# Optimization experiments

Measured on AMD Instinct MI355X. Metric: run time of the kernel, lower is better.

The kernel has to match this reference:

```python
import jax, jax.numpy as jnp
import numpy as np
from math import sqrt, ceil

OUTPUT_DIM = 50257
INPUT_DIM = 1024
N_CLASSES = int(ceil(sqrt(OUTPUT_DIM)))            # 225
N_OUT_PER_CLASS = int(ceil(OUTPUT_DIM / N_CLASSES))  # 224


def setup_inputs() -> dict:
    key = jax.random.key(0)
    k_x, k_w1, k_w2 = jax.random.split(key, 3)
    X = jax.random.normal(k_x, (8, 128, INPUT_DIM), dtype=jnp.float32)
    # glorot-ish scale so softmax logits stay in a sane range
    s1 = float(np.sqrt(2.0 / (INPUT_DIM + N_CLASSES)))
    s2 = float(np.sqrt(2.0 / (INPUT_DIM + N_OUT_PER_CLASS)))
    W1 = jax.random.normal(k_w1, (INPUT_DIM, N_CLASSES), dtype=jnp.float32) * s1
    b1 = jnp.zeros((N_CLASSES,), dtype=jnp.float32)
    W2 = jax.random.normal(k_w2, (N_CLASSES, INPUT_DIM, N_OUT_PER_CLASS), dtype=jnp.float32) * s2
    b2 = jnp.zeros((N_CLASSES, N_OUT_PER_CLASS), dtype=jnp.float32)
    return {"X": X, "W1": W1, "b1": b1, "W2": W2, "b2": b2}


def reference(X, W1, b1, W2, b2):
    """Two-level hierarchical softmax, inference path (target=None).

    P(y) = softmax(x@W1+b1)[class(y)] * softmax(x@W2[class(y)]+b2[class(y)])[offset(y)]
    Computed densely over all classes and flattened to the full vocab.
    """
    B, L, D = X.shape
    x = X.reshape(-1, D)                                    # [N, D], N = B*L
    class_probs = jax.nn.softmax(x @ W1 + b1, axis=-1)      # [N, C]
    # per-class logits: [N, C, O]
    acts = jnp.einsum('nd,cdo->nco', x, W2) + b2
    within = jax.nn.softmax(acts, axis=-1)                  # [N, C, O]
    probs = within * class_probs[:, :, None]                # [N, C, O]
    probs = probs.reshape(x.shape[0], N_CLASSES * N_OUT_PER_CLASS)[:, :OUTPUT_DIM]
    return probs.reshape(B, L, OUTPUT_DIM)
```

## Files before the change

### kernel.cpp

```cpp
#include <hip/hip_runtime.h>
#include <hip/hip_bf16.h>

#define CLS 225
#define OPC 224
#define DIM 1024
#define NTOK 1024
#define VOCAB 50257

#define BM 128
#define BK 32
#define NT 14

typedef __attribute__((ext_vector_type(8))) short bf16x8;
typedef __attribute__((ext_vector_type(4))) float f32x4;

__device__ __forceinline__ unsigned short f2bf(float f) {
  unsigned u = __float_as_uint(f);
  u += 0x7FFFu + ((u >> 16) & 1u);
  return (unsigned short)(u >> 16);
}

__device__ __forceinline__ void gll16(const void* gsrc, void* ldst) {
  __builtin_amdgcn_global_load_lds(
      (const __attribute__((address_space(1))) void*)gsrc,
      (__attribute__((address_space(3))) void*)ldst, 16, 0, 0);
}

__global__ __launch_bounds__(256) void hs_cls_fused(
    const float* __restrict__ X, const float* __restrict__ W1,
    const float* __restrict__ b1, float* __restrict__ cls,
    unsigned short* __restrict__ Xws)
{
  const int r0 = blockIdx.x * 4;
  const int tid = threadIdx.x;

  __shared__ float xs[4][DIM];
  __shared__ float lg[4][CLS];

  {
    const float4* src = (const float4*)(X + (size_t)r0 * DIM);
    float4* dst = (float4*)xs;
    for (int i = tid; i < 4 * DIM / 4; i += 256) dst[i] = src[i];
  }
  __syncthreads();

  for (int i = tid; i < 512; i += 256) {
    const int r = i >> 7, grp = i & 127;
    const int t = grp >> 2, slot = grp & 3;
    const int n = r0 + r;
    const float* p = &xs[r][t * 32 + slot * 8];
    bf16x8 pk;
#pragma unroll
    for (int j = 0; j < 8; ++j) pk[j] = (short)f2bf(p[j]);
    const int wb = (n * 64 + slot * 16) ^ ((n & 7) << 4);
    *(bf16x8*)((char*)Xws + (size_t)t * 65536 + wb) = pk;
  }

  if (tid < CLS) {
    float acc0 = 0.f, acc1 = 0.f, acc2 = 0.f, acc3 = 0.f;
    const float* w1p = W1 + tid;
    for (int d = 0; d < DIM; d += 8) {
      float w[8];
#pragma unroll
      for (int u = 0; u < 8; ++u) w[u] = w1p[(size_t)(d + u) * CLS];
#pragma unroll
      for (int u = 0; u < 8; ++u) {
        acc0 += xs[0][d + u] * w[u];
        acc1 += xs[1][d + u] * w[u];
        acc2 += xs[2][d + u] * w[u];
        acc3 += xs[3][d + u] * w[u];
      }
    }
    const float bb = b1[tid];
    lg[0][tid] = acc0 + bb;
    lg[1][tid] = acc1 + bb;
    lg[2][tid] = acc2 + bb;
    lg[3][tid] = acc3 + bb;
  }
  __syncthreads();

  const int wave = tid >> 6, lane = tid & 63;
  {
    const int r = wave;
    float v[4];
    float m = -1e30f;
#pragma unroll
    for (int i = 0; i < 4; ++i) {
      const int c2 = lane + i * 64;
      v[i] = (c2 < CLS) ? lg[r][c2] : -1e30f;
      m = fmaxf(m, v[i]);
    }
#pragma unroll
    for (int mask = 32; mask >= 1; mask >>= 1) m = fmaxf(m, __shfl_xor(m, mask));
    float e[4];
    float s = 0.f;
#pragma unroll
    for (int i = 0; i < 4; ++i) {
      const int c2 = lane + i * 64;
      e[i] = (c2 < CLS) ? __expf(v[i] - m) : 0.f;
      s += e[i];
    }
#pragma unroll
    for (int mask = 32; mask >= 1; mask >>= 1) s += __shfl_xor(s, mask);
    const float inv = 1.f / s;
#pragma unroll
    for (int i = 0; i < 4; ++i) {
      const int c2 = lane + i * 64;
      if (c2 < CLS) cls[(size_t)(r0 + r) * CLS + c2] = e[i] * inv;
    }
  }
}

__global__ __launch_bounds__(256) void hs_cls_kernel(
    const float* __restrict__ X, const float* __restrict__ W1,
    const float* __restrict__ b1, float* __restrict__ cls)
{
  const int r0 = blockIdx.x * 4;
  const int tid = threadIdx.x;

  __shared__ float xs[4][DIM];
  __shared__ float lg[4][CLS];

  {
    const float4* src = (const float4*)(X + (size_t)r0 * DIM);
    float4* dst = (float4*)xs;
    for (int i = tid; i < 4 * DIM / 4; i += 256) dst[i] = src[i];
  }
  __syncthreads();

  if (tid < CLS) {
    float acc0 = 0.f, acc1 = 0.f, acc2 = 0.f, acc3 = 0.f;
    const float* w1p = W1 + tid;
    for (int d = 0; d < DIM; d += 8) {
      float w[8];
#pragma unroll
      for (int u = 0; u < 8; ++u) w[u] = w1p[(size_t)(d + u) * CLS];
#pragma unroll
      for (int u = 0; u < 8; ++u) {
        acc0 += xs[0][d + u] * w[u];
        acc1 += xs[1][d + u] * w[u];
        acc2 += xs[2][d + u] * w[u];
        acc3 += xs[3][d + u] * w[u];
      }
    }
    const float bb = b1[tid];
    lg[0][tid] = acc0 + bb;
    lg[1][tid] = acc1 + bb;
    lg[2][tid] = acc2 + bb;
    lg[3][tid] = acc3 + bb;
  }
  __syncthreads();

  const int wave = tid >> 6, lane = tid & 63;
  {
    const int r = wave;
    float v[4];
    float m = -1e30f;
#pragma unroll
    for (int i = 0; i < 4; ++i) {
      const int c2 = lane + i * 64;
      v[i] = (c2 < CLS) ? lg[r][c2] : -1e30f;
      m = fmaxf(m, v[i]);
    }
#pragma unroll
    for (int mask = 32; mask >= 1; mask >>= 1) m = fmaxf(m, __shfl_xor(m, mask));
    float e[4];
    float s = 0.f;
#pragma unroll
    for (int i = 0; i < 4; ++i) {
      const int c2 = lane + i * 64;
      e[i] = (c2 < CLS) ? __expf(v[i] - m) : 0.f;
      s += e[i];
    }
#pragma unroll
    for (int mask = 32; mask >= 1; mask >>= 1) s += __shfl_xor(s, mask);
    const float inv = 1.f / s;
#pragma unroll
    for (int i = 0; i < 4; ++i) {
      const int c2 = lane + i * 64;
      if (c2 < CLS) cls[(size_t)(r0 + r) * CLS + c2] = e[i] * inv;
    }
  }
}

__global__ __launch_bounds__(256) void w2_convert(
    const float* __restrict__ W2, unsigned short* __restrict__ W2ws)
{
  const int ct = blockIdx.x;
  const int c = ct >> 5, t = ct & 31;
  const float* src = W2 + ((size_t)c * DIM + (size_t)t * 32) * OPC;
  char* dst = (char*)(W2ws + (size_t)ct * (OPC * 32));
  for (int i = threadIdx.x; i < 896; i += 256) {
    const int o = i % OPC, slot = i / OPC;
    const float* p = src + (size_t)(slot * 8) * OPC + o;
    bf16x8 pk;
#pragma unroll
    for (int j = 0; j < 8; ++j) pk[j] = (short)f2bf(p[(size_t)j * OPC]);
    const int wb = (o * 64 + slot * 16) ^ ((o & 7) << 4);
    *(bf16x8*)(dst + wb) = pk;
  }
}

__global__ __launch_bounds__(256) void x_convert_linear(
    const float* __restrict__ X, unsigned short* __restrict__ Xbf)
{
  const int r0 = blockIdx.x * 16;
  for (int i = threadIdx.x; i < 16 * 128; i += 256) {
    const int r = i >> 7, grp = i & 127;
    const int n = r0 + r;
    const float* p = X + (size_t)n * DIM + grp * 8;
    bf16x8 pk;
#pragma unroll
    for (int j = 0; j < 8; ++j) pk[j] = (short)f2bf(p[j]);
    *(bf16x8*)(Xbf + (size_t)n * DIM + grp * 8) = pk;
  }
}

__global__ __launch_bounds__(256, 1) void hs_main2(
    const unsigned short* __restrict__ W2ws, const float* __restrict__ b2,
    const unsigned short* __restrict__ Xws, const float* __restrict__ cls,
    float* __restrict__ out)
{
  const int bid = blockIdx.x;
  const int g = bid >> 6;
  const int xcd = bid & 7;
  const int rt = (bid >> 3) & 7;
  const int c = g * 8 + xcd;
  if (c >= CLS) return;
  const int n0 = rt * BM;

  __shared__ __align__(16) char As[2][8192];
  __shared__ __align__(16) char Bs[2][16384];

  const int tid = threadIdx.x;
  const int wv = tid >> 6, lane = tid & 63;
  const int lo16 = lane & 15, hi4 = lane >> 4;
  const int loff = lane * 16;

  f32x4 acc[2][NT];
#pragma unroll
  for (int mt = 0; mt < 2; ++mt)
#pragma unroll
    for (int nt = 0; nt < NT; ++nt) acc[mt][nt] = (f32x4){0.f, 0.f, 0.f, 0.f};

  const char* asrc0 = (const char*)Xws + (size_t)n0 * 64;
  const char* bsrc0 = (const char*)W2ws + (size_t)c * 32 * 14336;

#define STAGE(buf, t)                                                          \
  {                                                                            \
    const char* asrc = asrc0 + (size_t)(t) * 65536;                            \
    const char* bsrc = bsrc0 + (size_t)(t) * 14336;                            \
    char* Ad = As[buf];                                                        \
    char* Bd = Bs[buf];                                                        \
    _Pragma("unroll")                                                          \
    for (int i = 0; i < 6; ++i) {                                              \
      const int s = wv * 6 + i;                                                \
      const char* gp = (s < 8) ? (asrc + s * 1024 + loff)                      \
                               : (bsrc + (s - 8) * 1024 + loff);               \
      char* lp = (s < 8) ? (Ad + s * 1024) : (Bd + (s - 8) * 1024);            \
      gll16(gp, lp);                                                           \
    }                                                                          \
  }

  STAGE(0, 0);
  __syncthreads();

  int cur = 0;
  for (int t = 0; t < 32; ++t) {
    if (t < 31) STAGE(cur ^ 1, t + 1);

    const char* Ac = As[cur];
    const char* Bc = Bs[cur];
    const int ra = wv * 32 + lo16;
    const int axor = (lo16 & 7) << 4;
    const bf16x8 a0 = *(const bf16x8*)(Ac + ((ra * 64 + hi4 * 16) ^ axor));
    const bf16x8 a1 = *(const bf16x8*)(Ac + (((ra + 16) * 64 + hi4 * 16) ^ axor));
#pragma unroll
    for (int nt = 0; nt < NT; ++nt) {
      const int o = nt * 16 + lo16;
      const bf16x8 b = *(const bf16x8*)(Bc + ((o * 64 + hi4 * 16) ^ ((o & 7) << 4)));
      acc[0][nt] = __builtin_amdgcn_mfma_f32_16x16x32_bf16(a0, b, acc[0][nt], 0, 0, 0);
      acc[1][nt] = __builtin_amdgcn_mfma_f32_16x16x32_bf16(a1, b, acc[1][nt], 0, 0, 0);
    }

    __syncthreads();
    cur ^= 1;
  }
#undef STAGE

  float b2v[NT];
#pragma unroll
  for (int nt = 0; nt < NT; ++nt) b2v[nt] = b2[c * OPC + nt * 16 + lo16];

#pragma unroll
  for (int mt = 0; mt < 2; ++mt) {
#pragma unroll
    for (int j = 0; j < 4; ++j) {
      const int n = n0 + wv * 32 + mt * 16 + hi4 * 4 + j;
      float vv[NT];
      float m = -1e30f;
#pragma unroll
      for (int nt = 0; nt < NT; ++nt) {
        vv[nt] = acc[mt][nt][j] + b2v[nt];
        m = fmaxf(m, vv[nt]);
      }
#pragma unroll
      for (int mask = 8; mask >= 1; mask >>= 1) m = fmaxf(m, __shfl_xor(m, mask));
      float s = 0.f;
#pragma unroll
      for (int nt = 0; nt < NT; ++nt) {
        vv[nt] = __expf(vv[nt] - m);
        s += vv[nt];
      }
#pragma unroll
      for (int mask = 8; mask >= 1; mask >>= 1) s += __shfl_xor(s, mask);
      const float scale = cls[(size_t)n * CLS + c] / s;
      const size_t rowbase = (size_t)n * VOCAB;
      const int colbase = c * OPC + lo16;
#pragma unroll
      for (int nt = 0; nt < NT; ++nt) {
        const int col = colbase + nt * 16;
        if (col < VOCAB)
          __builtin_nontemporal_store(vv[nt] * scale, out + rowbase + col);
      }
    }
  }
}

__global__ __launch_bounds__(256, 1) void hs_main_fallback(
    const float* __restrict__ W2, const float* __restrict__ b2,
    const unsigned short* __restrict__ Xbf, const float* __restrict__ cls,
    float* __restrict__ out)
{
  const int bid = blockIdx.x;
  const int g = bid >> 6;
  const int xcd = bid & 7;
  const int rt = (bid >> 3) & 7;
  const int c = g * 8 + xcd;
  if (c >= CLS) return;
  const int n0 = rt * BM;
  const float* __restrict__ W2c = W2 + (size_t)c * DIM * OPC;

  __shared__ __align__(16) char As[BM * BK * 2];
  __shared__ __align__(16) char Bs[OPC * BK * 2];

  const int tid = threadIdx.x;
  const int wv = tid >> 6, lane = tid & 63;
  const int lo16 = lane & 15, hi4 = lane >> 4;

  f32x4 acc[2][NT];
#pragma unroll
  for (int mt = 0; mt < 2; ++mt)
#pragma unroll
    for (int nt = 0; nt < NT; ++nt) acc[mt][nt] = (f32x4){0.f, 0.f, 0.f, 0.f};

  const int an0 = tid >> 2;
  const int akp = tid & 3;

  for (int k0 = 0; k0 < DIM; k0 += BK) {
    __syncthreads();
#pragma unroll
    for (int r = 0; r < 2; ++r) {
      const int n = an0 + r * 64;
      const uint4 raw = *(const uint4*)(Xbf + (size_t)(n0 + n) * DIM + k0 + akp * 8);
      const int wb = (n * 64 + akp * 16) ^ ((n & 7) << 4);
      *(uint4*)(As + wb) = raw;
    }
#pragma unroll
    for (int r = 0; r < 4; ++r) {
      const int t = tid + r * 256;
      if (t < 896) {
        const int o = t % OPC;
        const int kg = t / OPC;
        const float* p = W2c + (size_t)(k0 + kg * 8) * OPC + o;
        bf16x8 pk;
#pragma unroll
        for (int j = 0; j < 8; ++j) pk[j] = (short)f2bf(p[(size_t)j * OPC]);
        const int wb = (o * 64 + kg * 16) ^ ((o & 7) << 4);
        *(bf16x8*)(Bs + wb) = pk;
      }
    }
    __syncthreads();

    const int ra = wv * 32 + lo16;
    const int axor = (lo16 & 7) << 4;
    const bf16x8 a0 = *(const bf16x8*)(As + ((ra * 64 + hi4 * 16) ^ axor));
    const bf16x8 a1 = *(const bf16x8*)(As + (((ra + 16) * 64 + hi4 * 16) ^ axor));
#pragma unroll
    for (int nt = 0; nt < NT; ++nt) {
      const int o = nt * 16 + lo16;
      const bf16x8 b = *(const bf16x8*)(Bs + ((o * 64 + hi4 * 16) ^ ((o & 7) << 4)));
      acc[0][nt] = __builtin_amdgcn_mfma_f32_16x16x32_bf16(a0, b, acc[0][nt], 0, 0, 0);
      acc[1][nt] = __builtin_amdgcn_mfma_f32_16x16x32_bf16(a1, b, acc[1][nt], 0, 0, 0);
    }
  }

  float b2v[NT];
#pragma unroll
  for (int nt = 0; nt < NT; ++nt) b2v[nt] = b2[c * OPC + nt * 16 + lo16];

#pragma unroll
  for (int mt = 0; mt < 2; ++mt) {
#pragma unroll
    for (int j = 0; j < 4; ++j) {
      const int n = n0 + wv * 32 + mt * 16 + hi4 * 4 + j;
      float vv[NT];
      float m = -1e30f;
#pragma unroll
      for (int nt = 0; nt < NT; ++nt) {
        vv[nt] = acc[mt][nt][j] + b2v[nt];
        m = fmaxf(m, vv[nt]);
      }
#pragma unroll
      for (int mask = 8; mask >= 1; mask >>= 1) m = fmaxf(m, __shfl_xor(m, mask));
      float s = 0.f;
#pragma unroll
      for (int nt = 0; nt < NT; ++nt) {
        vv[nt] = __expf(vv[nt] - m);
        s += vv[nt];
      }
#pragma unroll
      for (int mask = 8; mask >= 1; mask >>= 1) s += __shfl_xor(s, mask);
      const float scale = cls[(size_t)n * CLS + c] / s;
      const size_t rowbase = (size_t)n * VOCAB;
      const int colbase = c * OPC + lo16;
#pragma unroll
      for (int nt = 0; nt < NT; ++nt) {
        const int col = colbase + nt * 16;
        if (col < VOCAB)
          __builtin_nontemporal_store(vv[nt] * scale, out + rowbase + col);
      }
    }
  }
}

extern "C" void kernel_launch(void* const* d_in, const int* in_sizes, int n_in,
                              void* d_out, int out_size, void* d_ws, size_t ws_size,
                              hipStream_t stream) {
  const float* X  = (const float*)d_in[0];
  const float* W1 = (const float*)d_in[1];
  const float* b1 = (const float*)d_in[2];
  const float* W2 = (const float*)d_in[3];
  const float* b2 = (const float*)d_in[4];
  float* out = (float*)d_out;

  const size_t W2WS = (size_t)CLS * DIM * OPC * 2;
  const size_t XWS  = (size_t)NTOK * DIM * 2;
  const size_t CLSZ = (size_t)NTOK * CLS * 4;

  if (ws_size >= W2WS + XWS + CLSZ) {
    unsigned short* W2ws = (unsigned short*)d_ws;
    unsigned short* Xws  = (unsigned short*)((char*)d_ws + W2WS);
    float* cls = (float*)((char*)d_ws + W2WS + XWS);

    w2_convert<<<CLS * 32, 256, 0, stream>>>(W2, W2ws);
    hs_cls_fused<<<NTOK / 4, 256, 0, stream>>>(X, W1, b1, cls, Xws);
    hs_main2<<<29 * 64, 256, 0, stream>>>(W2ws, b2, Xws, cls, out);
  } else {
    unsigned short* Xbf = (unsigned short*)d_ws;
    float* cls = (float*)((char*)d_ws + (size_t)NTOK * DIM * 2);

    x_convert_linear<<<NTOK / 16, 256, 0, stream>>>(X, Xbf);
    hs_cls_kernel<<<NTOK / 4, 256, 0, stream>>>(X, W1, b1, cls);
    hs_main_fallback<<<29 * 64, 256, 0, stream>>>(W2, b2, Xbf, cls, out);
  }
}
```

Measured before the change: 297.2 us.

## Prefetch two stages ahead with partial vmcnt waits in per-class GEMM

```diff
diff --git a/kernel.cpp b/kernel.cpp
--- a/kernel.cpp
+++ b/kernel.cpp
@@ -243,50 +243,62 @@
 #pragma unroll
     for (int nt = 0; nt < NT; ++nt) acc[mt][nt] = (f32x4){0.f, 0.f, 0.f, 0.f};
 
-  const char* asrc0 = (const char*)Xws + (size_t)n0 * 64;
-  const char* bsrc0 = (const char*)W2ws + (size_t)c * 32 * 14336;
-
+  const char* xb  = (const char*)Xws + (size_t)n0 * 64 + loff;
+  const char* wb2 = (const char*)W2ws + (size_t)c * 32 * 14336 + loff;
+#define SEGDEF(i)                                                              \
+  const int s_##i = wv * 6 + i;                                                \
+  const bool isA_##i = (s_##i < 8);                                            \
+  const char* g_##i = isA_##i ? (xb + s_##i * 1024) : (wb2 + (s_##i - 8) * 1024); \
+  const size_t gstr_##i = isA_##i ? 65536u : 14336u;                           \
+  const int ldo_##i = isA_##i ? s_##i * 1024 : (s_##i - 8) * 1024;
+  SEGDEF(0) SEGDEF(1) SEGDEF(2) SEGDEF(3) SEGDEF(4) SEGDEF(5)
+
+#define STG(i, buf, t)                                                         \
+  gll16(g_##i + (size_t)(t) * gstr_##i, (isA_##i ? As[buf] : Bs[buf]) + ldo_##i)
 #define STAGE(buf, t)                                                          \
+  { STG(0, buf, t); STG(1, buf, t); STG(2, buf, t); STG(3, buf, t);            \
+    STG(4, buf, t); STG(5, buf, t); }
+
+#define COMPUTE(buf)                                                           \
   {                                                                            \
-    const char* asrc = asrc0 + (size_t)(t) * 65536;                            \
-    const char* bsrc = bsrc0 + (size_t)(t) * 14336;                            \
-    char* Ad = As[buf];                                                        \
-    char* Bd = Bs[buf];                                                        \
+    const char* Ac = As[buf];                                                  \
+    const char* Bc = Bs[buf];                                                  \
+    const int ra = wv * 32 + lo16;                                             \
+    const int axor = (lo16 & 7) << 4;                                          \
+    const bf16x8 va0 = *(const bf16x8*)(Ac + ((ra * 64 + hi4 * 16) ^ axor));   \
+    const bf16x8 va1 = *(const bf16x8*)(Ac + (((ra + 16) * 64 + hi4 * 16) ^ axor)); \
     _Pragma("unroll")                                                          \
-    for (int i = 0; i < 6; ++i) {                                              \
-      const int s = wv * 6 + i;                                                \
-      const char* gp = (s < 8) ? (asrc + s * 1024 + loff)                      \
-                               : (bsrc + (s - 8) * 1024 + loff);               \
-      char* lp = (s < 8) ? (Ad + s * 1024) : (Bd + (s - 8) * 1024);            \
-      gll16(gp, lp);                                                           \
+    for (int nt = 0; nt < NT; ++nt) {                                          \
+      const int o = nt * 16 + lo16;                                            \
+      const bf16x8 vb = *(const bf16x8*)(Bc + ((o * 64 + hi4 * 16) ^ ((o & 7) << 4))); \
+      acc[0][nt] = __builtin_amdgcn_mfma_f32_16x16x32_bf16(va0, vb, acc[0][nt], 0, 0, 0); \
+      acc[1][nt] = __builtin_amdgcn_mfma_f32_16x16x32_bf16(va1, vb, acc[1][nt], 0, 0, 0); \
     }                                                                          \
   }
 
   STAGE(0, 0);
-  __syncthreads();
-
-  int cur = 0;
-  for (int t = 0; t < 32; ++t) {
-    if (t < 31) STAGE(cur ^ 1, t + 1);
-
-    const char* Ac = As[cur];
-    const char* Bc = Bs[cur];
-    const int ra = wv * 32 + lo16;
-    const int axor = (lo16 & 7) << 4;
-    const bf16x8 a0 = *(const bf16x8*)(Ac + ((ra * 64 + hi4 * 16) ^ axor));
-    const bf16x8 a1 = *(const bf16x8*)(Ac + (((ra + 16) * 64 + hi4 * 16) ^ axor));
-#pragma unroll
-    for (int nt = 0; nt < NT; ++nt) {
-      const int o = nt * 16 + lo16;
-      const bf16x8 b = *(const bf16x8*)(Bc + ((o * 64 + hi4 * 16) ^ ((o & 7) << 4)));
-      acc[0][nt] = __builtin_amdgcn_mfma_f32_16x16x32_bf16(a0, b, acc[0][nt], 0, 0, 0);
-      acc[1][nt] = __builtin_amdgcn_mfma_f32_16x16x32_bf16(a1, b, acc[1][nt], 0, 0, 0);
-    }
-
-    __syncthreads();
-    cur ^= 1;
-  }
+  STAGE(1, 1);
+
+  for (int t = 0; t < 31; ++t) {
+    asm volatile("s_waitcnt vmcnt(6)" ::: "memory");
+    __builtin_amdgcn_s_barrier();
+    __builtin_amdgcn_sched_barrier(0);
+
+    COMPUTE(t & 1);
+
+    __builtin_amdgcn_sched_barrier(0);
+    __builtin_amdgcn_s_barrier();
+    if (t < 30) STAGE(t & 1, t + 2);
+  }
+  asm volatile("s_waitcnt vmcnt(0)" ::: "memory");
+  __builtin_amdgcn_s_barrier();
+  __builtin_amdgcn_sched_barrier(0);
+  COMPUTE(1);
+
 #undef STAGE
+#undef STG
+#undef SEGDEF
+#undef COMPUTE
 
   float b2v[NT];
 #pragma unroll
```

After: 279.3 us. 1.06x faster.

## Load MFMA fragments directly from global with prepacked layout, drop LDS staging

Applied to the files above, without the earlier changes.

```diff
diff --git a/kernel.cpp b/kernel.cpp
--- a/kernel.cpp
+++ b/kernel.cpp
@@ -20,12 +20,6 @@
   return (unsigned short)(u >> 16);
 }
 
-__device__ __forceinline__ void gll16(const void* gsrc, void* ldst) {
-  __builtin_amdgcn_global_load_lds(
-      (const __attribute__((address_space(1))) void*)gsrc,
-      (__attribute__((address_space(3))) void*)ldst, 16, 0, 0);
-}
-
 __global__ __launch_bounds__(256) void hs_cls_fused(
     const float* __restrict__ X, const float* __restrict__ W1,
     const float* __restrict__ b1, float* __restrict__ cls,
@@ -46,14 +40,14 @@
 
   for (int i = tid; i < 512; i += 256) {
     const int r = i >> 7, grp = i & 127;
-    const int t = grp >> 2, slot = grp & 3;
+    const int t = grp >> 2, hi4 = grp & 3;
     const int n = r0 + r;
-    const float* p = &xs[r][t * 32 + slot * 8];
+    const float* p = &xs[r][t * 32 + hi4 * 8];
     bf16x8 pk;
 #pragma unroll
     for (int j = 0; j < 8; ++j) pk[j] = (short)f2bf(p[j]);
-    const int wb = (n * 64 + slot * 16) ^ ((n & 7) << 4);
-    *(bf16x8*)((char*)Xws + (size_t)t * 65536 + wb) = pk;
+    const size_t wb = ((size_t)((n >> 4) * 32 + t)) * 1024 + (size_t)(hi4 * 16 + (n & 15)) * 16;
+    *(bf16x8*)((char*)Xws + wb) = pk;
   }
 
   if (tid < CLS) {
@@ -189,15 +183,16 @@
   const int ct = blockIdx.x;
   const int c = ct >> 5, t = ct & 31;
   const float* src = W2 + ((size_t)c * DIM + (size_t)t * 32) * OPC;
-  char* dst = (char*)(W2ws + (size_t)ct * (OPC * 32));
+  char* dst = (char*)W2ws + (size_t)c * 458752 + (size_t)t * 14336;
   for (int i = threadIdx.x; i < 896; i += 256) {
-    const int o = i % OPC, slot = i / OPC;
-    const float* p = src + (size_t)(slot * 8) * OPC + o;
+    const int nt = i >> 6, l = i & 63;
+    const int o = nt * 16 + (l & 15);
+    const int kl = (l >> 4) * 8;
+    const float* p = src + (size_t)kl * OPC + o;
     bf16x8 pk;
 #pragma unroll
     for (int j = 0; j < 8; ++j) pk[j] = (short)f2bf(p[(size_t)j * OPC]);
-    const int wb = (o * 64 + slot * 16) ^ ((o & 7) << 4);
-    *(bf16x8*)(dst + wb) = pk;
+    *(bf16x8*)(dst + (size_t)(nt * 64 + l) * 16) = pk;
   }
 }
 
@@ -216,7 +211,7 @@
   }
 }
 
-__global__ __launch_bounds__(256, 1) void hs_main2(
+__global__ __launch_bounds__(256, 2) void hs_main3(
     const unsigned short* __restrict__ W2ws, const float* __restrict__ b2,
     const unsigned short* __restrict__ Xws, const float* __restrict__ cls,
     float* __restrict__ out)
@@ -229,99 +224,98 @@
   if (c >= CLS) return;
   const int n0 = rt * BM;
 
-  __shared__ __align__(16) char As[2][8192];
-  __shared__ __align__(16) char Bs[2][16384];
+  __shared__ float2 red[4][64];
 
   const int tid = threadIdx.x;
   const int wv = tid >> 6, lane = tid & 63;
   const int lo16 = lane & 15, hi4 = lane >> 4;
-  const int loff = lane * 16;
-
-  f32x4 acc[2][NT];
-#pragma unroll
-  for (int mt = 0; mt < 2; ++mt)
-#pragma unroll
-    for (int nt = 0; nt < NT; ++nt) acc[mt][nt] = (f32x4){0.f, 0.f, 0.f, 0.f};
-
-  const char* asrc0 = (const char*)Xws + (size_t)n0 * 64;
-  const char* bsrc0 = (const char*)W2ws + (size_t)c * 32 * 14336;
-
-#define STAGE(buf, t)                                                          \
-  {                                                                            \
-    const char* asrc = asrc0 + (size_t)(t) * 65536;                            \
-    const char* bsrc = bsrc0 + (size_t)(t) * 14336;                            \
-    char* Ad = As[buf];                                                        \
-    char* Bd = Bs[buf];                                                        \
-    _Pragma("unroll")                                                          \
-    for (int i = 0; i < 6; ++i) {                                              \
-      const int s = wv * 6 + i;                                                \
-      const char* gp = (s < 8) ? (asrc + s * 1024 + loff)                      \
-                               : (bsrc + (s - 8) * 1024 + loff);               \
-      char* lp = (s < 8) ? (Ad + s * 1024) : (Bd + (s - 8) * 1024);            \
-      gll16(gp, lp);                                                           \
-    }                                                                          \
-  }
-
-  STAGE(0, 0);
+  const int wr = wv >> 1, wc = wv & 1;
+
+  f32x4 acc[4][7];
+#pragma unroll
+  for (int m = 0; m < 4; ++m)
+#pragma unroll
+    for (int nt = 0; nt < 7; ++nt) acc[m][nt] = (f32x4){0.f, 0.f, 0.f, 0.f};
+
+  const char* aB = (const char*)Xws + ((size_t)(n0 >> 4) + wr * 4) * 32768 + (size_t)lane * 16;
+  const char* bB = (const char*)W2ws + (size_t)c * 458752 + (size_t)(wc * 7) * 1024 + (size_t)lane * 16;
+
+#define LDA(dst, t)                                                            \
+  { _Pragma("unroll") for (int m = 0; m < 4; ++m)                              \
+      dst[m] = *(const bf16x8*)(aB + m * 32768 + (t) * 1024); }
+#define LDB(dst, t)                                                            \
+  { _Pragma("unroll") for (int nt = 0; nt < 7; ++nt)                           \
+      dst[nt] = *(const bf16x8*)(bB + (t) * 14336 + nt * 1024); }
+#define STEP(Aa, Bb)                                                           \
+  { _Pragma("unroll") for (int nt = 0; nt < 7; ++nt)                           \
+      _Pragma("unroll") for (int m = 0; m < 4; ++m)                            \
+        acc[m][nt] = __builtin_amdgcn_mfma_f32_16x16x32_bf16(Aa[m], Bb[nt],    \
+                                                             acc[m][nt], 0, 0, 0); }
+
+  bf16x8 A0[4], A1[4], B0[7], B1[7];
+  LDA(A0, 0); LDB(B0, 0);
+#pragma unroll
+  for (int tt = 0; tt < 16; ++tt) {
+    LDA(A1, 2 * tt + 1); LDB(B1, 2 * tt + 1);
+    STEP(A0, B0);
+    if (tt < 15) { LDA(A0, 2 * tt + 2); LDB(B0, 2 * tt + 2); }
+    STEP(A1, B1);
+  }
+#undef LDA
+#undef LDB
+#undef STEP
+
+  float b2v[7];
+#pragma unroll
+  for (int nt = 0; nt < 7; ++nt) b2v[nt] = b2[c * OPC + wc * 112 + nt * 16 + lo16];
+
+  float pmx[4][4], psum[4][4];
+#pragma unroll
+  for (int m = 0; m < 4; ++m) {
+#pragma unroll
+    for (int j = 0; j < 4; ++j) {
+      float mx = -1e30f;
+#pragma unroll
+      for (int nt = 0; nt < 7; ++nt) {
+        acc[m][nt][j] += b2v[nt];
+        mx = fmaxf(mx, acc[m][nt][j]);
+      }
+#pragma unroll
+      for (int mask = 8; mask >= 1; mask >>= 1) mx = fmaxf(mx, __shfl_xor(mx, mask));
+      float s = 0.f;
+#pragma unroll
+      for (int nt = 0; nt < 7; ++nt) {
+        const float v = __expf(acc[m][nt][j] - mx);
+        acc[m][nt][j] = v;
+        s += v;
+      }
+#pragma unroll
+      for (int mask = 8; mask >= 1; mask >>= 1) s += __shfl_xor(s, mask);
+      pmx[m][j] = mx;
+      psum[m][j] = s;
+      if (lo16 == 0) red[wv][m * 16 + hi4 * 4 + j] = make_float2(mx, s);
+    }
+  }
   __syncthreads();
 
-  int cur = 0;
-  for (int t = 0; t < 32; ++t) {
-    if (t < 31) STAGE(cur ^ 1, t + 1);
-
-    const char* Ac = As[cur];
-    const char* Bc = Bs[cur];
-    const int ra = wv * 32 + lo16;
-    const int axor = (lo16 & 7) << 4;
-    const bf16x8 a0 = *(const bf16x8*)(Ac + ((ra * 64 + hi4 * 16) ^ axor));
-    const bf16x8 a1 = *(const bf16x8*)(Ac + (((ra + 16) * 64 + hi4 * 16) ^ axor));
-#pragma unroll
-    for (int nt = 0; nt < NT; ++nt) {
-      const int o = nt * 16 + lo16;
-      const bf16x8 b = *(const bf16x8*)(Bc + ((o * 64 + hi4 * 16) ^ ((o & 7) << 4)));
-      acc[0][nt] = __builtin_amdgcn_mfma_f32_16x16x32_bf16(a0, b, acc[0][nt], 0, 0, 0);
-      acc[1][nt] = __builtin_amdgcn_mfma_f32_16x16x32_bf16(a1, b, acc[1][nt], 0, 0, 0);
-    }
-
-    __syncthreads();
-    cur ^= 1;
-  }
-#undef STAGE
-
-  float b2v[NT];
-#pragma unroll
-  for (int nt = 0; nt < NT; ++nt) b2v[nt] = b2[c * OPC + nt * 16 + lo16];
-
-#pragma unroll
-  for (int mt = 0; mt < 2; ++mt) {
+#pragma unroll
+  for (int m = 0; m < 4; ++m) {
 #pragma unroll
     for (int j = 0; j < 4; ++j) {
-      const int n = n0 + wv * 32 + mt * 16 + hi4 * 4 + j;
-      float vv[NT];
-      float m = -1e30f;
-#pragma unroll
-      for (int nt = 0; nt < NT; ++nt) {
-        vv[nt] = acc[mt][nt][j] + b2v[nt];
-        m = fmaxf(m, vv[nt]);
-      }
-#pragma unroll
-      for (int mask = 8; mask >= 1; mask >>= 1) m = fmaxf(m, __shfl_xor(m, mask));
-      float s = 0.f;
-#pragma unroll
-      for (int nt = 0; nt < NT; ++nt) {
-        vv[nt] = __expf(vv[nt] - m);
-        s += vv[nt];
-      }
-#pragma unroll
-      for (int mask = 8; mask >= 1; mask >>= 1) s += __shfl_xor(s, mask);
-      const float scale = cls[(size_t)n * CLS + c] / s;
+      const int rloc = m * 16 + hi4 * 4 + j;
+      const float2 ot = red[wv ^ 1][rloc];
+      const float mx = pmx[m][j], s = psum[m][j];
+      const float gm = fmaxf(mx, ot.x);
+      const float stot = s * __expf(mx - gm) + ot.y * __expf(ot.x - gm);
+      const int n = n0 + wr * 64 + rloc;
+      const float scale = cls[(size_t)n * CLS + c] * __expf(mx - gm) / stot;
       const size_t rowbase = (size_t)n * VOCAB;
-      const int colbase = c * OPC + lo16;
-#pragma unroll
-      for (int nt = 0; nt < NT; ++nt) {
+      const int colbase = c * OPC + wc * 112 + lo16;
+#pragma unroll
+      for (int nt = 0; nt < 7; ++nt) {
         const int col = colbase + nt * 16;
         if (col < VOCAB)
-          __builtin_nontemporal_store(vv[nt] * scale, out + rowbase + col);
+          __builtin_nontemporal_store(acc[m][nt][j] * scale, out + rowbase + col);
       }
     }
   }
@@ -455,7 +449,7 @@
 
     w2_convert<<<CLS * 32, 256, 0, stream>>>(W2, W2ws);
     hs_cls_fused<<<NTOK / 4, 256, 0, stream>>>(X, W1, b1, cls, Xws);
-    hs_main2<<<29 * 64, 256, 0, stream>>>(W2ws, b2, Xws, cls, out);
+    hs_main3<<<29 * 64, 256, 0, stream>>>(W2ws, b2, Xws, cls, out);
   } else {
     unsigned short* Xbf = (unsigned short*)d_ws;
     float* cls = (float*)((char*)d_ws + (size_t)NTOK * DIM * 2);
```

Result: slower. 414.9 us (+39.6%).
